# Kernel optimization log

Hardware: AMD Instinct MI355X
Metric: run time of the kernel (lower is better)

Reference implementation:

```python
import jax, jax.numpy as jnp
import numpy as np

# static config (matches init_kwargs)
T = 4            # number of block shape types
N_PER = 512      # blocks per type (sorted by type)
BLOCK_DIM = 32
OBST_DIM = 16
TGT_DIM = 16
HID = 128
HEADS = 4
ROUNDS = 3
N_OBS = 1024
N_TGT = 1023
GROUND_ACT = 8
BLOCK_ACT = 4 * 2  # n_receiving_faces * num_block_actions_per_face


def setup_inputs() -> dict:
    key = jax.random.key(0)
    ks = jax.random.split(key, 32)

    def rnd(i, shape, fan_in=None):
        s = 1.0 if fan_in is None else 1.0 / np.sqrt(fan_in)
        return (jax.random.normal(ks[i], shape, jnp.float32) * s).astype(jnp.float32)

    blocks_feat = rnd(0, (T * N_PER, BLOCK_DIM))
    type_col = jnp.repeat(jnp.arange(T), N_PER).astype(jnp.float32)[:, None]
    blocks = jnp.concatenate([blocks_feat, type_col], axis=1)  # [2048, 33]
    obstacles = rnd(1, (N_OBS, OBST_DIM))
    targets = rnd(2, (N_TGT, TGT_DIM))

    return dict(
        blocks=blocks, obstacles=obstacles, targets=targets,
        # per-type block encoders (stacked)
        Wb1=rnd(3, (T, BLOCK_DIM, HID), BLOCK_DIM), bb1=jnp.zeros((T, HID), jnp.float32),
        Wb2=rnd(4, (T, HID, HID), HID), bb2=jnp.zeros((T, HID), jnp.float32),
        # per-type block decoders (stacked)
        Wd=rnd(5, (T, 2 * HID, BLOCK_ACT), 2 * HID), bd=jnp.zeros((T, BLOCK_ACT), jnp.float32),
        # obstacle encoder
        Wo1=rnd(6, (OBST_DIM, HID), OBST_DIM), bo1=jnp.zeros((HID,), jnp.float32),
        Wo2=rnd(7, (HID, HID), HID), bo2=jnp.zeros((HID,), jnp.float32),
        # target encoder
        Wt1=rnd(8, (TGT_DIM, HID), TGT_DIM), bt1=jnp.zeros((HID,), jnp.float32),
        Wt2=rnd(9, (HID, HID), HID), bt2=jnp.zeros((HID,), jnp.float32),
        # ground param
        ground_param=(2.0 * jax.random.uniform(ks[10], (HID,), jnp.float32) - 1.0),
        # attention layer
        Wk=rnd(11, (HEADS, HID, HID), HID), Wq=rnd(12, (HEADS, HID, HID), HID),
        Wv=rnd(13, (HEADS, HID, HID), HID), Wm=jnp.ones((HEADS,), jnp.float32),
        Wg=rnd(14, (HID, HID), HID), bg=jnp.zeros((HID,), jnp.float32),
        # global + ground decoders
        Wglob=rnd(15, (HID, HID), HID), bglob=jnp.zeros((HID,), jnp.float32),
        Wgr=rnd(16, (2 * HID, GROUND_ACT), 2 * HID), bgr=jnp.zeros((GROUND_ACT,), jnp.float32),
    )


def _mlp2(x, W1, b1, W2, b2):
    return jax.nn.relu(x @ W1 + b1) @ W2 + b2


def reference(blocks, obstacles, targets, Wb1, bb1, Wb2, bb2, Wd, bd,
              Wo1, bo1, Wo2, bo2, Wt1, bt1, Wt2, bt2, ground_param,
              Wk, Wq, Wv, Wm, Wg, bg, Wglob, bglob, Wgr, bgr):
    # per-type block encoding (blocks sorted by type, equal counts -> static reshape)
    bf = blocks[:, :BLOCK_DIM].reshape(T, N_PER, BLOCK_DIM)
    h = jax.nn.relu(jnp.einsum('tnd,tdh->tnh', bf, Wb1) + bb1[:, None, :])
    xb = (jnp.einsum('tnh,thk->tnk', h, Wb2) + bb2[:, None, :]).reshape(T * N_PER, HID)
    xo = _mlp2(obstacles, Wo1, bo1, Wo2, bo2)
    xt = _mlp2(targets, Wt1, bt1, Wt2, bt2)
    x = jnp.concatenate([ground_param[None, :], xb, xo, xt], axis=0)  # [N, HID]

    for _ in range(ROUNDS):
        k = jnp.einsum('nd,hde->hne', x, Wk)
        q = jnp.einsum('nd,hde->hne', x, Wq)
        v = jnp.einsum('nd,hde->hne', x, Wv)
        e = jnp.einsum('hne,hme->hnm', q, k)           # [H, N, N]
        att = jax.nn.softmax(e, axis=-1)
        out = jnp.einsum('h,hnm,hme->ne', Wm, att, v)  # head-weighted sum
        x = x + jax.nn.relu((x + out) @ Wg + bg)

    G = x.mean(axis=0) @ Wglob + bglob                 # [HID]
    q_ground = jnp.concatenate([x[0], G]) @ Wgr + bgr  # [GROUND_ACT]

    xb2 = x[1:1 + T * N_PER].reshape(T, N_PER, HID)
    feat = jnp.concatenate([xb2, jnp.broadcast_to(G, (T, N_PER, HID))], axis=-1)
    q_blocks = jnp.einsum('tnf,tfa->tna', feat, Wd) + bd[:, None, :]  # [T, N_PER, 8]
    return q_ground, q_blocks
```

## Files before the change

### kernel.cpp

```cpp
#include <hip/hip_runtime.h>

#define HID 128
#define NNODES 4096
#define T 4
#define N_PER 512
#define NSPLIT 3

typedef unsigned short u16;
typedef __attribute__((ext_vector_type(8))) short bf16x8;
typedef __attribute__((ext_vector_type(4))) float f32x4;

#define MFMA(a, b, c) __builtin_amdgcn_mfma_f32_16x16x32_bf16((a), (b), (c), 0, 0, 0)

__device__ __forceinline__ u16 bfhi(float f) {
  union { float f; unsigned u; } v; v.f = f;
  return (u16)(v.u >> 16);
}
__device__ __forceinline__ float bff(u16 h) {
  union { float f; unsigned u; } v; v.u = ((unsigned)h) << 16;
  return v.f;
}

__global__ __launch_bounds__(128) void encode_kernel(
    const float* __restrict__ blocks, const float* __restrict__ obstacles,
    const float* __restrict__ targets,
    const float* __restrict__ Wb1, const float* __restrict__ bb1,
    const float* __restrict__ Wb2, const float* __restrict__ bb2,
    const float* __restrict__ Wo1, const float* __restrict__ bo1,
    const float* __restrict__ Wo2, const float* __restrict__ bo2,
    const float* __restrict__ Wt1, const float* __restrict__ bt1,
    const float* __restrict__ Wt2, const float* __restrict__ bt2,
    const float* __restrict__ ground, float* __restrict__ x) {
  int n = blockIdx.x;
  int j = threadIdx.x;
  __shared__ float in_s[32];
  __shared__ float h_s[128];
  if (n == 0) {
    x[j] = ground[j];
    return;
  }
  const float *W1, *b1, *W2, *b2, *inp;
  int D;
  if (n <= 2048) {
    int b = n - 1;
    int t = b >> 9;
    inp = blocks + (size_t)b * 33;
    D = 32;
    W1 = Wb1 + (size_t)t * 32 * HID;
    b1 = bb1 + (size_t)t * HID;
    W2 = Wb2 + (size_t)t * HID * HID;
    b2 = bb2 + (size_t)t * HID;
  } else if (n <= 3072) {
    int o = n - 2049;
    inp = obstacles + (size_t)o * 16;
    D = 16;
    W1 = Wo1; b1 = bo1; W2 = Wo2; b2 = bo2;
  } else {
    int tg = n - 3073;
    inp = targets + (size_t)tg * 16;
    D = 16;
    W1 = Wt1; b1 = bt1; W2 = Wt2; b2 = bt2;
  }
  if (j < D) in_s[j] = inp[j];
  __syncthreads();
  float acc = b1[j];
  for (int d = 0; d < D; d++) acc += in_s[d] * W1[d * HID + j];
  h_s[j] = fmaxf(acc, 0.f);
  __syncthreads();
  float acc2 = b2[j];
  for (int k = 0; k < HID; k++) acc2 += h_s[k] * W2[k * HID + j];
  x[(size_t)n * HID + j] = acc2;
}

__global__ __launch_bounds__(256) void qkv_kernel(
    const float* __restrict__ x, const float* __restrict__ Wk,
    const float* __restrict__ Wq, const float* __restrict__ Wv,
    u16* __restrict__ khi, u16* __restrict__ klo,
    u16* __restrict__ qhi, u16* __restrict__ qlo,
    u16* __restrict__ vthi, u16* __restrict__ vtlo) {
  int m = blockIdx.x;
  int h = m & 3;
  int sel = m >> 2;
  const float* W = (sel == 0 ? Wk : (sel == 1 ? Wq : Wv)) + (size_t)h * HID * HID;
  int r0 = blockIdx.y * 32;
  __shared__ float xs[32][132];
  int t = threadIdx.x;
  for (int i = t; i < 32 * 32; i += 256) {
    int r = i >> 5, c = (i & 31) * 4;
    *(float4*)&xs[r][c] = *(const float4*)(x + (size_t)(r0 + r) * HID + c);
  }
  __syncthreads();
  int j = t & 127;
  int rh = t >> 7;
  float acc[16];
#pragma unroll
  for (int i = 0; i < 16; i++) acc[i] = 0.f;
  for (int d = 0; d < HID; d += 4) {
    float w0 = W[(d + 0) * HID + j];
    float w1 = W[(d + 1) * HID + j];
    float w2 = W[(d + 2) * HID + j];
    float w3 = W[(d + 3) * HID + j];
#pragma unroll
    for (int i = 0; i < 16; i++) {
      float4 xv = *(const float4*)&xs[rh * 16 + i][d];
      acc[i] = fmaf(xv.x, w0, fmaf(xv.y, w1, fmaf(xv.z, w2, fmaf(xv.w, w3, acc[i]))));
    }
  }
  if (sel == 2) {
    __align__(16) u16 hb[16], lb[16];
#pragma unroll
    for (int i = 0; i < 16; i++) {
      float v = acc[i];
      u16 hi = bfhi(v);
      hb[i] = hi;
      lb[i] = bfhi(v - bff(hi));
    }
    u16* dh = vthi + ((size_t)(h * HID + j)) * NNODES + r0 + rh * 16;
    u16* dl = vtlo + ((size_t)(h * HID + j)) * NNODES + r0 + rh * 16;
    *(bf16x8*)dh = *(const bf16x8*)hb;
    *(bf16x8*)(dh + 8) = *(const bf16x8*)(hb + 8);
    *(bf16x8*)dl = *(const bf16x8*)lb;
    *(bf16x8*)(dl + 8) = *(const bf16x8*)(lb + 8);
  } else {
    u16* oh = (sel == 0 ? khi : qhi);
    u16* ol = (sel == 0 ? klo : qlo);
#pragma unroll
    for (int i = 0; i < 16; i++) {
      int row = r0 + rh * 16 + i;
      float v = acc[i];
      u16 hi = bfhi(v);
      oh[((size_t)h * NNODES + row) * HID + j] = hi;
      ol[((size_t)h * NNODES + row) * HID + j] = bfhi(v - bff(hi));
    }
  }
}

__global__ __launch_bounds__(256) void attn_kernel(
    const u16* __restrict__ qhi, const u16* __restrict__ qlo,
    const u16* __restrict__ khi, const u16* __restrict__ klo,
    const u16* __restrict__ vthi, const u16* __restrict__ vtlo,
    float* __restrict__ U, float* __restrict__ ml) {
  int h = blockIdx.x;
  int q0 = blockIdx.y * 64;
  int sp = blockIdx.z;
  int ktb = sp * 43;
  int kte = (sp == NSPLIT - 1) ? (NNODES / 32) : (ktb + 43);
  __shared__ __align__(16) u16 Kls[2][32 * 136];
  __shared__ __align__(16) u16 Vls[2][128 * 40];
  __shared__ __align__(16) u16 Pls[4][2][16 * 40];
  int t = threadIdx.x;
  int w = t >> 6;
  int l = t & 63;
  int lr = l & 15;
  int lg = l >> 4;

  int qrow = q0 + w * 16 + lr;
  const u16* qbh = qhi + ((size_t)h * NNODES + qrow) * HID + lg * 8;
  const u16* qbl = qlo + ((size_t)h * NNODES + qrow) * HID + lg * 8;
  bf16x8 qfh[4], qfl[4];
#pragma unroll
  for (int c = 0; c < 4; c++) {
    qfh[c] = *(const bf16x8*)(qbh + c * 32);
    qfl[c] = *(const bf16x8*)(qbl + c * 32);
  }

  f32x4 out[8];
#pragma unroll
  for (int i = 0; i < 8; i++) out[i] = (f32x4){0.f, 0.f, 0.f, 0.f};
  float run_m[4], run_l[4];
#pragma unroll
  for (int r = 0; r < 4; r++) { run_m[r] = -1e30f; run_l[r] = 0.f; }

  const u16* kbh = khi + (size_t)h * NNODES * HID;
  const u16* kbl = klo + (size_t)h * NNODES * HID;
  const u16* vbh = vthi + (size_t)h * HID * NNODES;
  const u16* vbl = vtlo + (size_t)h * HID * NNODES;

  for (int kt = ktb; kt < kte; kt++) {
#pragma unroll
    for (int i = 0; i < 2; i++) {
      int flat = i * 256 + t;
      int node = flat >> 4, ch = flat & 15;
      *(bf16x8*)&Kls[0][node * 136 + ch * 8] =
          *(const bf16x8*)(kbh + ((size_t)(kt * 32 + node)) * HID + ch * 8);
      *(bf16x8*)&Kls[1][node * 136 + ch * 8] =
          *(const bf16x8*)(kbl + ((size_t)(kt * 32 + node)) * HID + ch * 8);
      int d = flat >> 2, c2 = flat & 3;
      *(bf16x8*)&Vls[0][d * 40 + c2 * 8] =
          *(const bf16x8*)(vbh + (size_t)d * NNODES + kt * 32 + c2 * 8);
      *(bf16x8*)&Vls[1][d * 40 + c2 * 8] =
          *(const bf16x8*)(vbl + (size_t)d * NNODES + kt * 32 + c2 * 8);
    }
    __syncthreads();

    f32x4 ehh[2], ehl[2], elh[2];
#pragma unroll
    for (int ti = 0; ti < 2; ti++) {
      ehh[ti] = (f32x4){0.f, 0.f, 0.f, 0.f};
      ehl[ti] = (f32x4){0.f, 0.f, 0.f, 0.f};
      elh[ti] = (f32x4){0.f, 0.f, 0.f, 0.f};
    }
#pragma unroll
    for (int c = 0; c < 4; c++) {
#pragma unroll
      for (int ti = 0; ti < 2; ti++) {
        bf16x8 bh = *(const bf16x8*)&Kls[0][(ti * 16 + lr) * 136 + c * 32 + lg * 8];
        bf16x8 bl = *(const bf16x8*)&Kls[1][(ti * 16 + lr) * 136 + c * 32 + lg * 8];
        ehh[ti] = MFMA(qfh[c], bh, ehh[ti]);
        ehl[ti] = MFMA(qfh[c], bl, ehl[ti]);
        elh[ti] = MFMA(qfl[c], bh, elh[ti]);
      }
    }
    f32x4 e0 = ehh[0] + ehl[0] + elh[0];
    f32x4 e1 = ehh[1] + ehl[1] + elh[1];

    float sc[4];
#pragma unroll
    for (int r = 0; r < 4; r++) {
      float m2 = fmaxf(e0[r], e1[r]);
      m2 = fmaxf(m2, __shfl_xor(m2, 1));
      m2 = fmaxf(m2, __shfl_xor(m2, 2));
      m2 = fmaxf(m2, __shfl_xor(m2, 4));
      m2 = fmaxf(m2, __shfl_xor(m2, 8));
      float nm = fmaxf(run_m[r], m2);
      sc[r] = __expf(run_m[r] - nm);
      run_m[r] = nm;
      float p0 = __expf(e0[r] - nm);
      float p1 = __expf(e1[r] - nm);
      float lt = p0 + p1;
      lt += __shfl_xor(lt, 1);
      lt += __shfl_xor(lt, 2);
      lt += __shfl_xor(lt, 4);
      lt += __shfl_xor(lt, 8);
      run_l[r] = run_l[r] * sc[r] + lt;
      int prow = 4 * lg + r;
      u16 p0h = bfhi(p0);
      u16 p1h = bfhi(p1);
      Pls[w][0][prow * 40 + lr] = p0h;
      Pls[w][0][prow * 40 + 16 + lr] = p1h;
      Pls[w][1][prow * 40 + lr] = bfhi(p0 - bff(p0h));
      Pls[w][1][prow * 40 + 16 + lr] = bfhi(p1 - bff(p1h));
    }
#pragma unroll
    for (int dt = 0; dt < 8; dt++) {
      out[dt][0] *= sc[0];
      out[dt][1] *= sc[1];
      out[dt][2] *= sc[2];
      out[dt][3] *= sc[3];
    }

    bf16x8 ah = *(const bf16x8*)&Pls[w][0][lr * 40 + lg * 8];
    bf16x8 al = *(const bf16x8*)&Pls[w][1][lr * 40 + lg * 8];
#pragma unroll
    for (int dt = 0; dt < 8; dt++) {
      bf16x8 bh = *(const bf16x8*)&Vls[0][(dt * 16 + lr) * 40 + lg * 8];
      bf16x8 bl = *(const bf16x8*)&Vls[1][(dt * 16 + lr) * 40 + lg * 8];
      out[dt] = MFMA(ah, bh, out[dt]);
      out[dt] = MFMA(ah, bl, out[dt]);
      out[dt] = MFMA(al, bh, out[dt]);
    }
    __syncthreads();
  }

  float* ob = U + (((size_t)(sp * 4 + h) * NNODES) + q0 + w * 16) * HID;
#pragma unroll
  for (int dt = 0; dt < 8; dt++)
#pragma unroll
    for (int r = 0; r < 4; r++)
      ob[(size_t)(4 * lg + r) * HID + dt * 16 + lr] = out[dt][r];
  if (lr == 0) {
#pragma unroll
    for (int r = 0; r < 4; r++) {
      size_t mi = (((size_t)(sp * 4 + h) * NNODES) + q0 + w * 16 + 4 * lg + r) * 2;
      ml[mi] = run_m[r];
      ml[mi + 1] = run_l[r];
    }
  }
}

__global__ __launch_bounds__(256) void gate_kernel(
    float* __restrict__ x, const float* __restrict__ U,
    const float* __restrict__ ml,
    const float* __restrict__ Wm, const float* __restrict__ Wg,
    const float* __restrict__ bg) {
  int r0 = blockIdx.x * 32;
  __shared__ float ss[32][132];
  __shared__ float cs[32][4][NSPLIT];
  int t = threadIdx.x;
  if (t < 128) {
    int r = t >> 2, h = t & 3;
    int row = r0 + r;
    float ms[NSPLIT], ls[NSPLIT];
#pragma unroll
    for (int s = 0; s < NSPLIT; s++) {
      size_t mi = (((size_t)(s * 4 + h) * NNODES) + row) * 2;
      ms[s] = ml[mi];
      ls[s] = ml[mi + 1];
    }
    float M = fmaxf(fmaxf(ms[0], ms[1]), ms[2]);
    float w0 = __expf(ms[0] - M), w1 = __expf(ms[1] - M), w2 = __expf(ms[2] - M);
    float denom = ls[0] * w0 + ls[1] * w1 + ls[2] * w2;
    float wmh = Wm[h] / denom;
    cs[r][h][0] = w0 * wmh;
    cs[r][h][1] = w1 * wmh;
    cs[r][h][2] = w2 * wmh;
  }
  __syncthreads();
  for (int i = t; i < 32 * 32; i += 256) {
    int r = i >> 5, c = (i & 31) * 4;
    size_t off = (size_t)(r0 + r) * HID + c;
    float4 s = *(const float4*)(x + off);
#pragma unroll
    for (int h = 0; h < 4; h++) {
#pragma unroll
      for (int sp = 0; sp < NSPLIT; sp++) {
        float cc = cs[r][h][sp];
        float4 u = *(const float4*)(U + (size_t)(sp * 4 + h) * NNODES * HID + off);
        s.x = fmaf(cc, u.x, s.x);
        s.y = fmaf(cc, u.y, s.y);
        s.z = fmaf(cc, u.z, s.z);
        s.w = fmaf(cc, u.w, s.w);
      }
    }
    *(float4*)&ss[r][c] = s;
  }
  __syncthreads();
  int j = t & 127;
  int rh = t >> 7;
  float acc[16];
#pragma unroll
  for (int i = 0; i < 16; i++) acc[i] = bg[j];
  for (int d = 0; d < HID; d += 4) {
    float w0 = Wg[(d + 0) * HID + j];
    float w1 = Wg[(d + 1) * HID + j];
    float w2 = Wg[(d + 2) * HID + j];
    float w3 = Wg[(d + 3) * HID + j];
#pragma unroll
    for (int i = 0; i < 16; i++) {
      float4 sv = *(const float4*)&ss[rh * 16 + i][d];
      acc[i] = fmaf(sv.x, w0, fmaf(sv.y, w1, fmaf(sv.z, w2, fmaf(sv.w, w3, acc[i]))));
    }
  }
#pragma unroll
  for (int i = 0; i < 16; i++) {
    size_t r = (size_t)(r0 + rh * 16 + i) * HID + j;
    x[r] = x[r] + fmaxf(acc[i], 0.f);
  }
}

__global__ __launch_bounds__(128) void colsum_kernel(const float* __restrict__ x,
                                                     float* __restrict__ xsum) {
  int j = threadIdx.x;
  int r0 = blockIdx.x * 32;
  float s = 0.f;
  for (int r = 0; r < 32; r++) s += x[(size_t)(r0 + r) * HID + j];
  atomicAdd(&xsum[j], s);
}

__global__ __launch_bounds__(128) void ground_kernel(
    const float* __restrict__ x, const float* __restrict__ xsum,
    const float* __restrict__ Wglob, const float* __restrict__ bglob,
    const float* __restrict__ Wgr, const float* __restrict__ bgr,
    float* __restrict__ G, float* __restrict__ dout) {
  __shared__ float xm[128];
  __shared__ float Gs[128];
  int j = threadIdx.x;
  xm[j] = xsum[j] * (1.f / 4096.f);
  __syncthreads();
  float acc = bglob[j];
  for (int d = 0; d < 128; d++) acc += xm[d] * Wglob[d * 128 + j];
  G[j] = acc;
  Gs[j] = acc;
  __syncthreads();
  if (j < 8) {
    float a = bgr[j];
    for (int d = 0; d < 128; d++) a += x[d] * Wgr[d * 8 + j];
    for (int d = 0; d < 128; d++) a += Gs[d] * Wgr[(128 + d) * 8 + j];
    dout[j] = a;
  }
}

__global__ __launch_bounds__(256) void qblocks_kernel(
    const float* __restrict__ x, const float* __restrict__ G,
    const float* __restrict__ Wd, const float* __restrict__ bd,
    float* __restrict__ dout) {
  int r0 = blockIdx.x * 32;
  int tt = r0 >> 9;
  __shared__ float xs[32][132];
  __shared__ float Gs[128];
  int t = threadIdx.x;
  if (t < 128) Gs[t] = G[t];
  for (int i = t; i < 32 * 32; i += 256) {
    int r = i >> 5, c = (i & 31) * 4;
    *(float4*)&xs[r][c] = *(const float4*)(x + (size_t)(1 + r0 + r) * HID + c);
  }
  __syncthreads();
  int r = t >> 3, a = t & 7;
  const float* Wt = Wd + (size_t)tt * 256 * 8;
  float acc = bd[tt * 8 + a];
  for (int d = 0; d < 128; d++) acc += xs[r][d] * Wt[d * 8 + a];
  for (int d = 0; d < 128; d++) acc += Gs[d] * Wt[(128 + d) * 8 + a];
  dout[8 + (size_t)(r0 + r) * 8 + a] = acc;
}

extern "C" void kernel_launch(void* const* d_in, const int* in_sizes, int n_in,
                              void* d_out, int out_size, void* d_ws, size_t ws_size,
                              hipStream_t stream) {
  const float* blocks    = (const float*)d_in[0];
  const float* obstacles = (const float*)d_in[1];
  const float* targets   = (const float*)d_in[2];
  const float* Wb1 = (const float*)d_in[3];
  const float* bb1 = (const float*)d_in[4];
  const float* Wb2 = (const float*)d_in[5];
  const float* bb2 = (const float*)d_in[6];
  const float* Wd  = (const float*)d_in[7];
  const float* bd  = (const float*)d_in[8];
  const float* Wo1 = (const float*)d_in[9];
  const float* bo1 = (const float*)d_in[10];
  const float* Wo2 = (const float*)d_in[11];
  const float* bo2 = (const float*)d_in[12];
  const float* Wt1 = (const float*)d_in[13];
  const float* bt1 = (const float*)d_in[14];
  const float* Wt2 = (const float*)d_in[15];
  const float* bt2 = (const float*)d_in[16];
  const float* ground = (const float*)d_in[17];
  const float* Wk = (const float*)d_in[18];
  const float* Wq = (const float*)d_in[19];
  const float* Wv = (const float*)d_in[20];
  const float* Wm = (const float*)d_in[21];
  const float* Wg = (const float*)d_in[22];
  const float* bg = (const float*)d_in[23];
  const float* Wglob = (const float*)d_in[24];
  const float* bglob = (const float*)d_in[25];
  const float* Wgr = (const float*)d_in[26];
  const float* bgr = (const float*)d_in[27];

  float* ws = (float*)d_ws;
  float* x    = ws;
  float* U    = x + 524288;
  float* ml   = U + (size_t)NSPLIT * 4 * NNODES * HID;
  float* xsum = ml + (size_t)NSPLIT * 4 * NNODES * 2;
  float* G    = xsum + 128;
  u16* qhi  = (u16*)(G + 128);
  u16* qlo  = qhi + 2097152;
  u16* khi  = qlo + 2097152;
  u16* klo  = khi + 2097152;
  u16* vthi = klo + 2097152;
  u16* vtlo = vthi + 2097152;
  float* dout = (float*)d_out;

  encode_kernel<<<NNODES, 128, 0, stream>>>(
      blocks, obstacles, targets, Wb1, bb1, Wb2, bb2, Wo1, bo1, Wo2, bo2,
      Wt1, bt1, Wt2, bt2, ground, x);

  for (int round = 0; round < 3; round++) {
    qkv_kernel<<<dim3(12, NNODES / 32), 256, 0, stream>>>(
        x, Wk, Wq, Wv, khi, klo, qhi, qlo, vthi, vtlo);
    attn_kernel<<<dim3(4, NNODES / 64, NSPLIT), 256, 0, stream>>>(
        qhi, qlo, khi, klo, vthi, vtlo, U, ml);
    gate_kernel<<<NNODES / 32, 256, 0, stream>>>(x, U, ml, Wm, Wg, bg);
  }

  hipMemsetAsync(xsum, 0, 128 * sizeof(float), stream);
  colsum_kernel<<<NNODES / 32, 128, 0, stream>>>(x, xsum);
  ground_kernel<<<1, 128, 0, stream>>>(x, xsum, Wglob, bglob, Wgr, bgr, G, dout);
  qblocks_kernel<<<64, 256, 0, stream>>>(x, G, Wd, bd, dout);
}
```

Measured before the change: 867.8 us.

## Move QKV projection to split-bf16 MFMA with pre-split weights and activations

Replaces the FP32 scalar-FMA QKV projection with a 16x16x32 bf16 MFMA kernel that uses three products per tile (hi*hi, hi*lo, lo*hi) to keep near-FP32 accuracy. The Wk/Wq/Wv weights are split into transposed hi/lo bf16 copies once per call, and the encode and gate kernels now also write hi/lo bf16 copies of x for the MFMA inputs. This targets the scalar FLOP cost of the projection. In exchange it adds extra global writes in encode and gate, a presplit kernel launch, and scattered 2-byte output stores, most notably for the transposed V.

After: 858.1 us. Within noise of the previous version (-1.1%).

```diff
diff --git a/kernel.cpp b/kernel.cpp
--- a/kernel.cpp
+++ b/kernel.cpp
@@ -19,6 +19,23 @@
 __device__ __forceinline__ float bff(u16 h) {
   union { float f; unsigned u; } v; v.u = ((unsigned)h) << 16;
   return v.f;
+}
+
+__global__ __launch_bounds__(256) void presplit_kernel(
+    const float* __restrict__ Wk, const float* __restrict__ Wq,
+    const float* __restrict__ Wv,
+    u16* __restrict__ wthi, u16* __restrict__ wtlo) {
+  int t = blockIdx.x * 256 + threadIdx.x;
+  int m = t >> 14;
+  int rem = t & 16383;
+  int k = rem >> 7, col = rem & 127;
+  int h = m & 3, sel = m >> 2;
+  const float* W = (sel == 0 ? Wk : (sel == 1 ? Wq : Wv)) + (size_t)h * HID * HID;
+  float v = W[k * HID + col];
+  u16 hi = bfhi(v);
+  size_t o = (size_t)m * 16384 + col * 128 + k;
+  wthi[o] = hi;
+  wtlo[o] = bfhi(v - bff(hi));
 }
 
 __global__ __launch_bounds__(128) void encode_kernel(
@@ -30,13 +47,18 @@
     const float* __restrict__ Wo2, const float* __restrict__ bo2,
     const float* __restrict__ Wt1, const float* __restrict__ bt1,
     const float* __restrict__ Wt2, const float* __restrict__ bt2,
-    const float* __restrict__ ground, float* __restrict__ x) {
+    const float* __restrict__ ground, float* __restrict__ x,
+    u16* __restrict__ xhi, u16* __restrict__ xlo) {
   int n = blockIdx.x;
   int j = threadIdx.x;
   __shared__ float in_s[32];
   __shared__ float h_s[128];
   if (n == 0) {
-    x[j] = ground[j];
+    float g = ground[j];
+    x[j] = g;
+    u16 hi = bfhi(g);
+    xhi[j] = hi;
+    xlo[j] = bfhi(g - bff(hi));
     return;
   }
   const float *W1, *b1, *W2, *b2, *inp;
@@ -69,69 +91,68 @@
   __syncthreads();
   float acc2 = b2[j];
   for (int k = 0; k < HID; k++) acc2 += h_s[k] * W2[k * HID + j];
-  x[(size_t)n * HID + j] = acc2;
-}
-
-__global__ __launch_bounds__(256) void qkv_kernel(
-    const float* __restrict__ x, const float* __restrict__ Wk,
-    const float* __restrict__ Wq, const float* __restrict__ Wv,
+  size_t o = (size_t)n * HID + j;
+  x[o] = acc2;
+  u16 hi = bfhi(acc2);
+  xhi[o] = hi;
+  xlo[o] = bfhi(acc2 - bff(hi));
+}
+
+__global__ __launch_bounds__(64) void qkv_kernel(
+    const u16* __restrict__ xhi, const u16* __restrict__ xlo,
+    const u16* __restrict__ wthi, const u16* __restrict__ wtlo,
     u16* __restrict__ khi, u16* __restrict__ klo,
     u16* __restrict__ qhi, u16* __restrict__ qlo,
     u16* __restrict__ vthi, u16* __restrict__ vtlo) {
   int m = blockIdx.x;
-  int h = m & 3;
-  int sel = m >> 2;
-  const float* W = (sel == 0 ? Wk : (sel == 1 ? Wq : Wv)) + (size_t)h * HID * HID;
-  int r0 = blockIdx.y * 32;
-  __shared__ float xs[32][132];
-  int t = threadIdx.x;
-  for (int i = t; i < 32 * 32; i += 256) {
-    int r = i >> 5, c = (i & 31) * 4;
-    *(float4*)&xs[r][c] = *(const float4*)(x + (size_t)(r0 + r) * HID + c);
-  }
-  __syncthreads();
-  int j = t & 127;
-  int rh = t >> 7;
-  float acc[16];
-#pragma unroll
-  for (int i = 0; i < 16; i++) acc[i] = 0.f;
-  for (int d = 0; d < HID; d += 4) {
-    float w0 = W[(d + 0) * HID + j];
-    float w1 = W[(d + 1) * HID + j];
-    float w2 = W[(d + 2) * HID + j];
-    float w3 = W[(d + 3) * HID + j];
-#pragma unroll
-    for (int i = 0; i < 16; i++) {
-      float4 xv = *(const float4*)&xs[rh * 16 + i][d];
-      acc[i] = fmaf(xv.x, w0, fmaf(xv.y, w1, fmaf(xv.z, w2, fmaf(xv.w, w3, acc[i]))));
+  int h = m & 3, sel = m >> 2;
+  int r0 = blockIdx.y * 16;
+  int l = threadIdx.x;
+  int lr = l & 15, lg = l >> 4;
+  const u16* wh = wthi + (size_t)m * 16384;
+  const u16* wl = wtlo + (size_t)m * 16384;
+  f32x4 acc[8];
+#pragma unroll
+  for (int i = 0; i < 8; i++) acc[i] = (f32x4){0.f, 0.f, 0.f, 0.f};
+#pragma unroll
+  for (int c = 0; c < 4; c++) {
+    bf16x8 ah = *(const bf16x8*)(xhi + (size_t)(r0 + lr) * HID + c * 32 + lg * 8);
+    bf16x8 al = *(const bf16x8*)(xlo + (size_t)(r0 + lr) * HID + c * 32 + lg * 8);
+#pragma unroll
+    for (int dt = 0; dt < 8; dt++) {
+      bf16x8 bh = *(const bf16x8*)(wh + (dt * 16 + lr) * 128 + c * 32 + lg * 8);
+      bf16x8 bl = *(const bf16x8*)(wl + (dt * 16 + lr) * 128 + c * 32 + lg * 8);
+      acc[dt] = MFMA(ah, bh, acc[dt]);
+      acc[dt] = MFMA(ah, bl, acc[dt]);
+      acc[dt] = MFMA(al, bh, acc[dt]);
     }
   }
   if (sel == 2) {
-    __align__(16) u16 hb[16], lb[16];
-#pragma unroll
-    for (int i = 0; i < 16; i++) {
-      float v = acc[i];
-      u16 hi = bfhi(v);
-      hb[i] = hi;
-      lb[i] = bfhi(v - bff(hi));
-    }
-    u16* dh = vthi + ((size_t)(h * HID + j)) * NNODES + r0 + rh * 16;
-    u16* dl = vtlo + ((size_t)(h * HID + j)) * NNODES + r0 + rh * 16;
-    *(bf16x8*)dh = *(const bf16x8*)hb;
-    *(bf16x8*)(dh + 8) = *(const bf16x8*)(hb + 8);
-    *(bf16x8*)dl = *(const bf16x8*)lb;
-    *(bf16x8*)(dl + 8) = *(const bf16x8*)(lb + 8);
+#pragma unroll
+    for (int dt = 0; dt < 8; dt++)
+#pragma unroll
+      for (int r = 0; r < 4; r++) {
+        int row = r0 + 4 * lg + r, col = dt * 16 + lr;
+        float v = acc[dt][r];
+        u16 hi = bfhi(v);
+        size_t o = ((size_t)h * HID + col) * NNODES + row;
+        vthi[o] = hi;
+        vtlo[o] = bfhi(v - bff(hi));
+      }
   } else {
     u16* oh = (sel == 0 ? khi : qhi);
     u16* ol = (sel == 0 ? klo : qlo);
 #pragma unroll
-    for (int i = 0; i < 16; i++) {
-      int row = r0 + rh * 16 + i;
-      float v = acc[i];
-      u16 hi = bfhi(v);
-      oh[((size_t)h * NNODES + row) * HID + j] = hi;
-      ol[((size_t)h * NNODES + row) * HID + j] = bfhi(v - bff(hi));
-    }
+    for (int dt = 0; dt < 8; dt++)
+#pragma unroll
+      for (int r = 0; r < 4; r++) {
+        int row = r0 + 4 * lg + r, col = dt * 16 + lr;
+        float v = acc[dt][r];
+        u16 hi = bfhi(v);
+        size_t o = ((size_t)h * NNODES + row) * HID + col;
+        oh[o] = hi;
+        ol[o] = bfhi(v - bff(hi));
+      }
   }
 }
 
@@ -282,7 +303,8 @@
     float* __restrict__ x, const float* __restrict__ U,
     const float* __restrict__ ml,
     const float* __restrict__ Wm, const float* __restrict__ Wg,
-    const float* __restrict__ bg) {
+    const float* __restrict__ bg,
+    u16* __restrict__ xhi, u16* __restrict__ xlo) {
   int r0 = blockIdx.x * 32;
   __shared__ float ss[32][132];
   __shared__ float cs[32][4][NSPLIT];
@@ -344,7 +366,11 @@
 #pragma unroll
   for (int i = 0; i < 16; i++) {
     size_t r = (size_t)(r0 + rh * 16 + i) * HID + j;
-    x[r] = x[r] + fmaxf(acc[i], 0.f);
+    float nv = x[r] + fmaxf(acc[i], 0.f);
+    x[r] = nv;
+    u16 hi = bfhi(nv);
+    xhi[r] = hi;
+    xlo[r] = bfhi(nv - bff(hi));
   }
 }
 
@@ -438,8 +464,8 @@
   float* ws = (float*)d_ws;
   float* x    = ws;
   float* U    = x + 524288;
-  float* ml   = U + (size_t)NSPLIT * 4 * NNODES * HID;
-  float* xsum = ml + (size_t)NSPLIT * 4 * NNODES * 2;
+  float* ml   = U + 6291456;
+  float* xsum = ml + 98304;
   float* G    = xsum + 128;
   u16* qhi  = (u16*)(G + 128);
   u16* qlo  = qhi + 2097152;
@@ -447,18 +473,23 @@
   u16* klo  = khi + 2097152;
   u16* vthi = klo + 2097152;
   u16* vtlo = vthi + 2097152;
+  u16* xhi  = vtlo + 2097152;
+  u16* xlo  = xhi + 524288;
+  u16* wthi = xlo + 524288;
+  u16* wtlo = wthi + 196608;
   float* dout = (float*)d_out;
 
+  presplit_kernel<<<768, 256, 0, stream>>>(Wk, Wq, Wv, wthi, wtlo);
   encode_kernel<<<NNODES, 128, 0, stream>>>(
       blocks, obstacles, targets, Wb1, bb1, Wb2, bb2, Wo1, bo1, Wo2, bo2,
-      Wt1, bt1, Wt2, bt2, ground, x);
+      Wt1, bt1, Wt2, bt2, ground, x, xhi, xlo);
 
   for (int round = 0; round < 3; round++) {
-    qkv_kernel<<<dim3(12, NNODES / 32), 256, 0, stream>>>(
-        x, Wk, Wq, Wv, khi, klo, qhi, qlo, vthi, vtlo);
+    qkv_kernel<<<dim3(12, NNODES / 16), 64, 0, stream>>>(
+        xhi, xlo, wthi, wtlo, khi, klo, qhi, qlo, vthi, vtlo);
     attn_kernel<<<dim3(4, NNODES / 64, NSPLIT), 256, 0, stream>>>(
         qhi, qlo, khi, klo, vthi, vtlo, U, ml);
-    gate_kernel<<<NNODES / 32, 256, 0, stream>>>(x, U, ml, Wm, Wg, bg);
+    gate_kernel<<<NNODES / 32, 256, 0, stream>>>(x, U, ml, Wm, Wg, bg, xhi, xlo);
   }
 
   hipMemsetAsync(xsum, 0, 128 * sizeof(float), stream);
```
